# Kernel tuning notes

Hardware: AMD Instinct MI355X
Metric: run time of the kernel (lower is better)

The kernel has to match this reference:

```python
import jax, jax.numpy as jnp
import numpy as np

B, T, D_MODEL, H, RPR_K = 2, 2048, 1024, 16, 8
DK = D_MODEL // H  # 64
NUM_RPR = 2 * RPR_K + 1


def setup_inputs() -> dict:
    key = jax.random.key(0)
    ks = jax.random.split(key, 16)
    s = 0.02
    inp = {
        "query": jax.random.normal(ks[0], (B, T, D_MODEL), jnp.float32),
        "key": jax.random.normal(ks[1], (B, T, D_MODEL), jnp.float32),
        "value": jax.random.normal(ks[2], (B, T, D_MODEL), jnp.float32),
        "mask": jnp.ones((B, 1, 1, T), dtype=bool),
        "w_q": jax.random.normal(ks[3], (D_MODEL, H * DK), jnp.float32) * s,
        "b_q": jnp.zeros((H * DK,), jnp.float32),
        "w_k": jax.random.normal(ks[4], (D_MODEL, H * DK), jnp.float32) * s,
        "b_k": jnp.zeros((H * DK,), jnp.float32),
        "w_v": jax.random.normal(ks[5], (D_MODEL, H * DK), jnp.float32) * s,
        "b_v": jnp.zeros((H * DK,), jnp.float32),
        "w_o": jax.random.normal(ks[6], (H * DK, D_MODEL), jnp.float32) * s,
        "b_o": jnp.zeros((D_MODEL,), jnp.float32),
        "rpr_key_table": jax.random.normal(ks[7], (NUM_RPR, DK), jnp.float32),
        "rpr_value_table": jax.random.normal(ks[8], (NUM_RPR, DK), jnp.float32),
    }
    return inp


def _rel_edges(seq_len):
    # edges[i, j] = clamp(j - i + rpr_k, 0, 2*rpr_k)  -> [T, T] int32
    seq = jnp.arange(seq_len)
    edges = seq[None, :] - seq[:, None] + RPR_K
    return jnp.clip(edges, 0, 2 * RPR_K)


def reference(query, key, value, mask, w_q, b_q, w_k, b_k, w_v, b_v,
              w_o, b_o, rpr_key_table, rpr_value_table):
    Bsz, Tlen, _ = query.shape
    edges = _rel_edges(Tlen)                       # [T, T]
    ek = rpr_key_table[edges]                      # [T, T, DK]
    ev = rpr_value_table[edges]                    # [T, T, DK]

    def proj(x, w, b):
        return (x @ w + b).reshape(Bsz, Tlen, H, DK).transpose(0, 2, 1, 3)  # [B,H,T,DK]

    q = proj(query, w_q, b_q)
    k = proj(key, w_k, b_k)
    v = proj(value, w_v, b_v)

    scores_qk = jnp.einsum('bhtd,bhsd->bhts', q, k)
    scores_qek = jnp.einsum('bhtd,tsd->bhts', q, ek)
    scores = (scores_qk + scores_qek) / jnp.sqrt(jnp.float32(DK))
    scores = jnp.where(mask, scores, jnp.float32(-1e9))
    a = jax.nn.softmax(scores, axis=-1)            # [B,H,T,T]

    upd = jnp.einsum('bhts,bhsd->bhtd', a, v)
    upd_e = jnp.einsum('bhts,tsd->bhtd', a, ev)
    x = (upd + upd_e).transpose(0, 2, 1, 3).reshape(Bsz, Tlen, H * DK)
    return x @ w_o + b_o
```

## Files before the change

### kernel.cpp

```cpp
#include <hip/hip_runtime.h>
#include <stdint.h>


typedef unsigned short u16;
typedef __attribute__((ext_vector_type(4))) float f32x4;
typedef __attribute__((ext_vector_type(4))) int   i32x4;
typedef __attribute__((ext_vector_type(8))) __bf16 bh8;
typedef __attribute__((ext_vector_type(4))) __bf16 bh4;

#define T_LEN 2048
#define NHEAD 16
#define NR    17

#define SCALE_LOG2 0.18033688011112042f
#define CLAMP_LOG2 86.56170245333781f

__device__ __forceinline__ float bf2f(u16 x) {
  unsigned u = ((unsigned)x) << 16;
  return __builtin_bit_cast(float, u);
}
__device__ __forceinline__ u16 f2bf(float f) {
  unsigned u = __builtin_bit_cast(unsigned, f);
  u = u + 0x7fffu + ((u >> 16) & 1u);
  return (u16)(u >> 16);
}
__device__ __forceinline__ f32x4 zero4() { f32x4 z = {0.f, 0.f, 0.f, 0.f}; return z; }

__device__ __forceinline__ f32x4 mfma16(bh8 a, bh8 b, f32x4 c) {
  return __builtin_amdgcn_mfma_f32_16x16x32_bf16(a, b, c, 0, 0, 0);
}

__device__ __forceinline__ void bar_sync() {
  __builtin_amdgcn_sched_barrier(0);
  asm volatile("s_waitcnt lgkmcnt(0)" ::: "memory");
  __builtin_amdgcn_s_barrier();
  __builtin_amdgcn_sched_barrier(0);
}

__device__ __forceinline__ void wait_vm0() {
  __builtin_amdgcn_sched_barrier(0);
  asm volatile("s_waitcnt vmcnt(0)" ::: "memory");
  __builtin_amdgcn_sched_barrier(0);
}

__device__ __forceinline__ void async16(const u16* g, u16* l) {
  __builtin_amdgcn_global_load_lds(
      (const __attribute__((address_space(1))) void*)g,
      (__attribute__((address_space(3))) void*)l, 16, 0, 0);
}

__device__ __forceinline__ bh8 ldfrag(const u16* base, int row, int qc) {
  const i32x4 v = *(const i32x4*)(base + row * 64 + ((qc ^ (row & 7)) << 3));
  return __builtin_bit_cast(bh8, v);
}

__global__ __launch_bounds__(256) void prep_kernel(
    const float* __restrict__ xq, const float* __restrict__ xk,
    const float* __restrict__ xv, const float* __restrict__ w0,
    const float* __restrict__ w1, const float* __restrict__ w2,
    const float* __restrict__ w3, u16* __restrict__ oq, u16* __restrict__ ok,
    u16* __restrict__ ov, u16* __restrict__ t0, u16* __restrict__ t1,
    u16* __restrict__ t2, u16* __restrict__ t3) {
  __shared__ u16 tile[32][33];
  const int z = blockIdx.z;
  if (z < 3) {
    const float* S = (z == 0) ? xq : (z == 1) ? xk : xv;
    u16* D = (z == 0) ? oq : (z == 1) ? ok : ov;
    const size_t i = ((size_t)blockIdx.x * 256 + threadIdx.x) * 8;
    const f32x4 v0 = *(const f32x4*)(S + i);
    const f32x4 v1 = *(const f32x4*)(S + i + 4);
    u16 o[8];
#pragma unroll
    for (int j = 0; j < 4; ++j) {
      o[j] = f2bf(v0[j]);
      o[4 + j] = f2bf(v1[j]);
    }
    i32x4 w;
    __builtin_memcpy(&w, o, 16);
    *(i32x4*)(D + i) = w;
  } else {
    if (blockIdx.x >= 1024) return;
    const float* S = (z == 3) ? w0 : (z == 4) ? w1 : (z == 5) ? w2 : w3;
    u16* D = (z == 3) ? t0 : (z == 4) ? t1 : (z == 5) ? t2 : t3;
    const int tx = threadIdx.x & 31, ty = threadIdx.x >> 5;
    const int bx = blockIdx.x & 31, by = blockIdx.x >> 5;
#pragma unroll
    for (int i = 0; i < 4; ++i) {
      const int y = by * 32 + ty + i * 8;
      tile[ty + i * 8][tx] = f2bf(S[(size_t)y * 1024 + bx * 32 + tx]);
    }
    __syncthreads();
#pragma unroll
    for (int i = 0; i < 4; ++i) {
      const int y = bx * 32 + ty + i * 8;
      D[(size_t)y * 1024 + by * 32 + tx] = tile[tx][ty + i * 8];
    }
  }
}

__device__ __forceinline__ void gemm_body(const u16* __restrict__ A,
                                          const u16* __restrict__ Bm,
                                          const float* __restrict__ bias,
                                          void* __restrict__ out, int mode,
                                          int bm, int bn) {
  __shared__ __align__(16) u16 As[2][128 * 32];
  __shared__ __align__(16) u16 Bs[2][128 * 32];
  const int tid = threadIdx.x;
  const int wv = tid >> 6;
  const int ln = tid & 63;
  const int quad = ln >> 4, l15 = ln & 15;
  const int wr = wv >> 1, wc = wv & 1;

  f32x4 acc[4][4];
#pragma unroll
  for (int i = 0; i < 4; ++i)
#pragma unroll
    for (int j = 0; j < 4; ++j) acc[i][j] = zero4();

  const int c0 = tid, c1 = tid + 256;
  const size_t aoff0 = (size_t)(bm * 128 + (c0 >> 2)) * 1024 + (c0 & 3) * 8;
  const size_t aoff1 = (size_t)(bm * 128 + (c1 >> 2)) * 1024 + (c1 & 3) * 8;
  const size_t boff0 = (size_t)(bn * 128 + (c0 >> 2)) * 1024 + (c0 & 3) * 8;
  const size_t boff1 = (size_t)(bn * 128 + (c1 >> 2)) * 1024 + (c1 & 3) * 8;

  u16* ad0[2] = {&As[0][(wv * 64) * 8], &As[1][(wv * 64) * 8]};
  u16* ad1[2] = {&As[0][(256 + wv * 64) * 8], &As[1][(256 + wv * 64) * 8]};
  u16* bd0[2] = {&Bs[0][(wv * 64) * 8], &Bs[1][(wv * 64) * 8]};
  u16* bd1[2] = {&Bs[0][(256 + wv * 64) * 8], &Bs[1][(256 + wv * 64) * 8]};

  async16(A + aoff0, ad0[0]);
  async16(A + aoff1, ad1[0]);
  async16(Bm + boff0, bd0[0]);
  async16(Bm + boff1, bd1[0]);
  __syncthreads();

  for (int kt = 0; kt < 32; ++kt) {
    const int cur = kt & 1, nxt = cur ^ 1;
    if (kt < 31) {
      const int ko = (kt + 1) * 32;
      async16(A + aoff0 + ko, ad0[nxt]);
      async16(A + aoff1 + ko, ad1[nxt]);
      async16(Bm + boff0 + ko, bd0[nxt]);
      async16(Bm + boff1 + ko, bd1[nxt]);
    }

    bh8 af[4], bf[4];
#pragma unroll
    for (int mi = 0; mi < 4; ++mi)
      af[mi] = __builtin_bit_cast(
          bh8,
          *(const i32x4*)&As[cur][(wr * 64 + mi * 16 + l15) * 32 + quad * 8]);
#pragma unroll
    for (int ni = 0; ni < 4; ++ni)
      bf[ni] = __builtin_bit_cast(
          bh8,
          *(const i32x4*)&Bs[cur][(wc * 64 + ni * 16 + l15) * 32 + quad * 8]);
#pragma unroll
    for (int mi = 0; mi < 4; ++mi)
#pragma unroll
      for (int ni = 0; ni < 4; ++ni)
        acc[mi][ni] = mfma16(af[mi], bf[ni], acc[mi][ni]);

    __syncthreads();
  }

#pragma unroll
  for (int mi = 0; mi < 4; ++mi) {
    const int row0 = bm * 128 + wr * 64 + mi * 16 + quad * 4;
#pragma unroll
    for (int ni = 0; ni < 4; ++ni) {
      const int col = bn * 128 + wc * 64 + ni * 16 + l15;
      const float bcol = (mode == 3) ? 0.f : bias[col];
#pragma unroll
      for (int reg = 0; reg < 4; ++reg) {
        const int r = row0 + reg;
        const float v = acc[mi][ni][reg] + ((mode == 3) ? bias[r] : bcol);
        if (mode == 0) {
          ((float*)out)[(size_t)r * 1024 + col] = v;
        } else if (mode == 1) {
          const int bb = r >> 11, t = r & 2047;
          const int h = col >> 6, d = col & 63;
          ((u16*)out)[(((size_t)bb * NHEAD + h) * T_LEN + (size_t)t) * 64 + d] =
              f2bf(v);
        } else {
          const int h = r >> 6, d = r & 63;
          const int bb = col >> 11, t = col & 2047;
          ((u16*)out)[(((size_t)bb * NHEAD + h) * 64 + (size_t)d) * T_LEN + t] =
              f2bf(v);
        }
      }
    }
  }
}

__global__ __launch_bounds__(256) void gemm_qkv_kernel(
    const u16* __restrict__ xq, const u16* __restrict__ xk,
    const u16* __restrict__ xv, const u16* __restrict__ wtq,
    const u16* __restrict__ wtk, const u16* __restrict__ wtv,
    const float* __restrict__ bq, const float* __restrict__ bk,
    const float* __restrict__ bv, u16* __restrict__ oq, u16* __restrict__ ok,
    u16* __restrict__ ovt) {
  const int z = blockIdx.z;
  if (z == 0)
    gemm_body(xq, wtq, bq, oq, 1, blockIdx.x, blockIdx.y);
  else if (z == 1)
    gemm_body(xk, wtk, bk, ok, 1, blockIdx.x, blockIdx.y);
  else
    gemm_body(wtv, xv, bv, ovt, 3, blockIdx.y, blockIdx.x);
}

__global__ __launch_bounds__(256) void gemm_o_kernel(const u16* __restrict__ X,
                                                     const u16* __restrict__ Wt,
                                                     const float* __restrict__ bias,
                                                     float* __restrict__ out) {
  gemm_body(X, Wt, bias, out, 0, blockIdx.x, blockIdx.y);
}

__global__ __launch_bounds__(512) void attn_kernel(
    const u16* __restrict__ Qw, const u16* __restrict__ Kw,
    const u16* __restrict__ Vtw, const float* __restrict__ rkt,
    const float* __restrict__ rvt, u16* __restrict__ U) {
  __shared__ __align__(16) u16 smu[24576];
  __shared__ float smf[5120];
  u16* Qs = smu;
  u16* Ps = smu;
  float* qes = smf;
  float* aw = smf + 2176;
  float* lp = smf + 4352;
  float* s0p = smf + 4608;
  float* s16p = smf + 4864;
  float* rvs = (float*)(smu + 16384);

  const int tid = threadIdx.x;
  const int wv = tid >> 6, ln = tid & 63;
  const int tg = wv & 3, sh = wv >> 2;
  const int quad = ln >> 4, l15 = ln & 15;
  const int wg = blockIdx.x;
  const int xcd = wg & 7;
  const int slot = wg >> 3;
  const int qt = slot & 15;
  const int bh = xcd * 4 + (slot >> 4);
  const size_t hb = (size_t)bh * (T_LEN * 64);

  const int kr = tid >> 3;
  const int kgp = (tid & 7) ^ ((tid >> 3) & 7);
  const u16* ksrc = Kw + hb + (size_t)kr * 64 + kgp * 8;
  const u16* vsrc = Vtw + hb + (size_t)kr * T_LEN + kgp * 8;
  u16* const ldsK = smu + 8192 + wv * 512;
  u16* const ldsV = smu + 16384 + wv * 512;
  const int qrow = wv * 16 + ((ln >> 3) & 7);
  const int qgp = (ln & 7) ^ ((ln >> 3) & 7);
  const u16* qsrc = Qw + hb + (size_t)(qt * 128 + qrow) * 64 + qgp * 8;
  u16* const ldsQ = smu + wv * 1024;

  async16(qsrc, ldsQ);
  async16(qsrc + 512, ldsQ + 512);
  async16(ksrc, ldsK);
  async16(vsrc, ldsV);
  wait_vm0();
  bar_sync();

  for (int i = tid; i < 128 * NR; i += 512) {
    const int row = i / NR, r = i - row * NR;
    float s = 0.f;
#pragma unroll
    for (int c = 0; c < 8; ++c) {
      const i32x4 qv = *(const i32x4*)&Qs[row * 64 + ((c ^ (row & 7)) << 3)];
      const u16* qq = (const u16*)&qv;
#pragma unroll
      for (int j = 0; j < 8; ++j) s += bf2f(qq[j]) * rkt[r * 64 + c * 8 + j];
    }
    qes[i] = s;
    aw[i] = 0.f;
  }

  bh8 qf[2][2];
  const int row0 = tg * 32 + l15;
#pragma unroll
  for (int tt = 0; tt < 2; ++tt) {
    qf[tt][0] = ldfrag(Qs, row0 + tt * 16, quad);
    qf[tt][1] = ldfrag(Qs, row0 + tt * 16, quad + 4);
  }
  bar_sync();

  float qb0[2], qb16[2];
#pragma unroll
  for (int tt = 0; tt < 2; ++tt) {
    qb0[tt] = qes[(row0 + tt * 16) * NR + 0] * SCALE_LOG2;
    qb16[tt] = qes[(row0 + tt * 16) * NR + 16] * SCALE_LOG2;
  }

  float l_l[2] = {0.f, 0.f}, s0_l[2] = {0.f, 0.f}, s16_l[2] = {0.f, 0.f};
  f32x4 oacc[2][2];
#pragma unroll
  for (int tt = 0; tt < 2; ++tt)
#pragma unroll
    for (int ni = 0; ni < 2; ++ni) oacc[tt][ni] = zero4();

  for (int st = 0; st < 32; ++st) {
    const int cur = st & 1;
    const u16* Kc = smu + 8192 + cur * 4096;
    const u16* Vc = smu + 16384 + cur * 4096;
    if (st < 31) {
      const int nxt = cur ^ 1;
      async16(ksrc + (size_t)(st + 1) * 4096, ldsK + nxt * 4096);
      async16(vsrc + (size_t)(st + 1) * 64, ldsV + nxt * 4096);
    }

    __builtin_amdgcn_s_setprio(1);
#pragma unroll
    for (int m2 = 0; m2 < 2; ++m2) {
      const int srow = (sh * 2 + m2) * 16 + l15;
      const bh8 kf0 = ldfrag(Kc, srow, quad);
      const bh8 kf1 = ldfrag(Kc, srow, quad + 4);
#pragma unroll
      for (int tt = 0; tt < 2; ++tt) {
        f32x4 sacc = mfma16(kf0, qf[tt][0], zero4());
        sacc = mfma16(kf1, qf[tt][1], sacc);

        const int row = row0 + tt * 16;
        const int delta16 = st * 4 + sh * 2 + m2 - (qt * 8 + tg * 2 + tt);
        float p[4];
        if (delta16 < -1 || delta16 > 1) {
          const float qb = (delta16 < 0) ? qb0[tt] : qb16[tt];
          float ts = 0.f;
#pragma unroll
          for (int reg = 0; reg < 4; ++reg) {
            const float x = fminf(sacc[reg] * SCALE_LOG2 + qb, CLAMP_LOG2);
            const float pv = __builtin_amdgcn_exp2f(x);
            p[reg] = pv;
            ts += pv;
          }
          l_l[tt] += ts;
          if (delta16 < 0)
            s0_l[tt] += ts;
          else
            s16_l[tt] += ts;
        } else {
          const int base8 = delta16 * 16 + quad * 4 - l15 + 8;
#pragma unroll
          for (int reg = 0; reg < 4; ++reg) {
            int rel = base8 + reg;
            rel = rel < 0 ? 0 : (rel > 16 ? 16 : rel);
            const float x =
                fminf((sacc[reg] + qes[row * NR + rel]) * SCALE_LOG2,
                      CLAMP_LOG2);
            const float pv = __builtin_amdgcn_exp2f(x);
            p[reg] = pv;
            l_l[tt] += pv;
            if (rel == 0)
              s0_l[tt] += pv;
            else if (rel == 16)
              s16_l[tt] += pv;
            else
              atomicAdd(&aw[row * NR + rel], pv);
          }
        }

        bh4 pb = {(__bf16)p[0], (__bf16)p[1], (__bf16)p[2], (__bf16)p[3]};
        const int qc = 4 * sh + 2 * m2 + (quad >> 1);
        *(unsigned long long*)&Ps[row * 64 + ((qc ^ (row & 7)) << 3) +
                                  (quad & 1) * 4] =
            __builtin_bit_cast(unsigned long long, pb);
      }
    }

    bar_sync();

#pragma unroll
    for (int ks = 0; ks < 2; ++ks) {
      const int kc = ks * 4 + quad;
      const bh8 pf0 = ldfrag(Ps, row0, kc);
      const bh8 pf1 = ldfrag(Ps, row0 + 16, kc);
#pragma unroll
      for (int ni = 0; ni < 2; ++ni) {
        const bh8 vf = ldfrag(Vc, sh * 32 + ni * 16 + l15, kc);
        oacc[0][ni] = mfma16(pf0, vf, oacc[0][ni]);
        oacc[1][ni] = mfma16(pf1, vf, oacc[1][ni]);
      }
    }
    __builtin_amdgcn_s_setprio(0);

    wait_vm0();
    bar_sync();
  }

#pragma unroll
  for (int tt = 0; tt < 2; ++tt) {
    l_l[tt] += __shfl_xor(l_l[tt], 16);
    l_l[tt] += __shfl_xor(l_l[tt], 32);
    s0_l[tt] += __shfl_xor(s0_l[tt], 16);
    s0_l[tt] += __shfl_xor(s0_l[tt], 32);
    s16_l[tt] += __shfl_xor(s16_l[tt], 16);
    s16_l[tt] += __shfl_xor(s16_l[tt], 32);
    if (quad == 0) {
      lp[sh * 128 + row0 + tt * 16] = l_l[tt];
      s0p[sh * 128 + row0 + tt * 16] = s0_l[tt];
      s16p[sh * 128 + row0 + tt * 16] = s16_l[tt];
    }
  }
  for (int i = tid; i < NR * 64; i += 512) rvs[i] = rvt[i];
  __syncthreads();

  for (int i = tid; i < 128 * NR; i += 512) {
    const int row = i / NR, rr = i - row * NR;
    float v = aw[i];
    if (rr == 0) v += s0p[row] + s0p[128 + row];
    if (rr == 16) v += s16p[row] + s16p[128 + row];
    aw[i] = v;
  }
  if (tid < 128) lp[tid] += lp[128 + tid];
  __syncthreads();

  const int bb = bh >> 4, hh = bh & 15;
#pragma unroll
  for (int tt = 0; tt < 2; ++tt) {
#pragma unroll
    for (int ni = 0; ni < 2; ++ni) {
      const int d = sh * 32 + ni * 16 + l15;
#pragma unroll
      for (int reg = 0; reg < 4; ++reg) {
        const int rowi = tg * 32 + tt * 16 + quad * 4 + reg;
        float o = oacc[tt][ni][reg];
        float e = 0.f;
#pragma unroll
        for (int rr = 0; rr < NR; ++rr)
          e += aw[rowi * NR + rr] * rvs[rr * 64 + d];
        const float ov = (o + e) / lp[rowi];
        const int tgl = qt * 128 + rowi;
        U[((size_t)bb * T_LEN + tgl) * 1024 + hh * 64 + d] = f2bf(ov);
      }
    }
  }
}

extern "C" void kernel_launch(void* const* d_in, const int* in_sizes, int n_in,
                              void* d_out, int out_size, void* d_ws,
                              size_t ws_size, hipStream_t stream) {
  const float* query = (const float*)d_in[0];
  const float* key = (const float*)d_in[1];
  const float* value = (const float*)d_in[2];
  const float* w_q = (const float*)d_in[4];
  const float* b_q = (const float*)d_in[5];
  const float* w_k = (const float*)d_in[6];
  const float* b_k = (const float*)d_in[7];
  const float* w_v = (const float*)d_in[8];
  const float* b_v = (const float*)d_in[9];
  const float* w_o = (const float*)d_in[10];
  const float* b_o = (const float*)d_in[11];
  const float* rkt = (const float*)d_in[12];
  const float* rvt = (const float*)d_in[13];

  char* ws = (char*)d_ws;
  const size_t MB2 = 1u << 21, MB8 = 1u << 23;
  u16* wtq = (u16*)(ws + 0 * MB2);
  u16* wtk = (u16*)(ws + 1 * MB2);
  u16* wtv = (u16*)(ws + 2 * MB2);
  u16* wto = (u16*)(ws + 3 * MB2);
  u16* Xq = (u16*)(ws + 4 * MB2 + 0 * MB8);
  u16* Xk = (u16*)(ws + 4 * MB2 + 1 * MB8);
  u16* Xv = (u16*)(ws + 4 * MB2 + 2 * MB8);
  u16* Qw = (u16*)(ws + 4 * MB2 + 3 * MB8);
  u16* Kw = (u16*)(ws + 4 * MB2 + 4 * MB8);
  u16* Vtw = (u16*)(ws + 4 * MB2 + 5 * MB8);
  u16* Uw = (u16*)(ws + 4 * MB2 + 6 * MB8);

  prep_kernel<<<dim3(2048, 1, 7), 256, 0, stream>>>(
      query, key, value, w_q, w_k, w_v, w_o, Xq, Xk, Xv, wtq, wtk, wtv, wto);
  gemm_qkv_kernel<<<dim3(32, 8, 3), 256, 0, stream>>>(
      Xq, Xk, Xv, wtq, wtk, wtv, b_q, b_k, b_v, Qw, Kw, Vtw);
  attn_kernel<<<dim3(512), 512, 0, stream>>>(Qw, Kw, Vtw, rkt, rvt, Uw);
  gemm_o_kernel<<<dim3(32, 8), 256, 0, stream>>>(Uw, wto, b_o, (float*)d_out);
}
```

Measured before the change: 315.4 us.

## Restructure attention to 32x32 MFMA with register-resident P via permlane swap

The attention kernel moves from 512 threads using 16x16x32 MFMAs to 256 threads where each wave owns 32 query rows and computes the full 64-wide key block with 32x32x16 MFMAs. P is converted to bf16 with packed converts and rearranged across lane halves with v_permlane32_swap, so it feeds the PV MFMA directly from registers. This removes the LDS round trip for P and the mid-iteration barrier, and the cross-wave reduction of row sums. In exchange there are fewer waves per block, larger accumulators (more VGPR pressure) and more reliance on LDS async loads per wave.

```diff
diff --git a/kernel.cpp b/kernel.cpp
--- a/kernel.cpp
+++ b/kernel.cpp
@@ -4,9 +4,9 @@
 
 typedef unsigned short u16;
 typedef __attribute__((ext_vector_type(4))) float f32x4;
+typedef __attribute__((ext_vector_type(16))) float f32x16;
 typedef __attribute__((ext_vector_type(4))) int   i32x4;
 typedef __attribute__((ext_vector_type(8))) __bf16 bh8;
-typedef __attribute__((ext_vector_type(4))) __bf16 bh4;
 
 #define T_LEN 2048
 #define NHEAD 16
@@ -25,9 +25,23 @@
   return (u16)(u >> 16);
 }
 __device__ __forceinline__ f32x4 zero4() { f32x4 z = {0.f, 0.f, 0.f, 0.f}; return z; }
+__device__ __forceinline__ f32x16 zero16() {
+  f32x16 z = {0.f, 0.f, 0.f, 0.f, 0.f, 0.f, 0.f, 0.f,
+              0.f, 0.f, 0.f, 0.f, 0.f, 0.f, 0.f, 0.f};
+  return z;
+}
 
 __device__ __forceinline__ f32x4 mfma16(bh8 a, bh8 b, f32x4 c) {
   return __builtin_amdgcn_mfma_f32_16x16x32_bf16(a, b, c, 0, 0, 0);
+}
+__device__ __forceinline__ f32x16 mfma32(bh8 a, bh8 b, f32x16 c) {
+  return __builtin_amdgcn_mfma_f32_32x32x16_bf16(a, b, c, 0, 0, 0);
+}
+
+__device__ __forceinline__ unsigned cvtpk(float a, float b) {
+  unsigned r;
+  asm("v_cvt_pk_bf16_f32 %0, %1, %2" : "=v"(r) : "v"(a), "v"(b));
+  return r;
 }
 
 __device__ __forceinline__ void bar_sync() {
@@ -216,51 +230,55 @@
   gemm_body(X, Wt, bias, out, 0, blockIdx.x, blockIdx.y);
 }
 
-__global__ __launch_bounds__(512) void attn_kernel(
+__global__ __launch_bounds__(256) void attn_kernel(
     const u16* __restrict__ Qw, const u16* __restrict__ Kw,
     const u16* __restrict__ Vtw, const float* __restrict__ rkt,
     const float* __restrict__ rvt, u16* __restrict__ U) {
   __shared__ __align__(16) u16 smu[24576];
-  __shared__ float smf[5120];
-  u16* Qs = smu;
-  u16* Ps = smu;
-  float* qes = smf;
-  float* aw = smf + 2176;
-  float* lp = smf + 4352;
-  float* s0p = smf + 4608;
-  float* s16p = smf + 4864;
-  float* rvs = (float*)(smu + 16384);
+  __shared__ float smf[5568];
+  u16* const Qs = smu;
+  float* const qes = smf;
+  float* const aw = smf + 2176;
+  float* const lp = smf + 4352;
+  float* const rvs = smf + 4480;
 
   const int tid = threadIdx.x;
   const int wv = tid >> 6, ln = tid & 63;
-  const int tg = wv & 3, sh = wv >> 2;
-  const int quad = ln >> 4, l15 = ln & 15;
+  const int l31 = ln & 31, hi = ln >> 5;
   const int wg = blockIdx.x;
   const int xcd = wg & 7;
   const int slot = wg >> 3;
   const int qt = slot & 15;
   const int bh = xcd * 4 + (slot >> 4);
   const size_t hb = (size_t)bh * (T_LEN * 64);
-
-  const int kr = tid >> 3;
-  const int kgp = (tid & 7) ^ ((tid >> 3) & 7);
-  const u16* ksrc = Kw + hb + (size_t)kr * 64 + kgp * 8;
-  const u16* vsrc = Vtw + hb + (size_t)kr * T_LEN + kgp * 8;
-  u16* const ldsK = smu + 8192 + wv * 512;
-  u16* const ldsV = smu + 16384 + wv * 512;
-  const int qrow = wv * 16 + ((ln >> 3) & 7);
-  const int qgp = (ln & 7) ^ ((ln >> 3) & 7);
-  const u16* qsrc = Qw + hb + (size_t)(qt * 128 + qrow) * 64 + qgp * 8;
-  u16* const ldsQ = smu + wv * 1024;
-
-  async16(qsrc, ldsQ);
-  async16(qsrc + 512, ldsQ + 512);
-  async16(ksrc, ldsK);
-  async16(vsrc, ldsV);
+  const int t0 = qt * 128 + wv * 32;
+  const int tl = wv * 32 + l31;
+
+  const int r8 = ln >> 3, c8 = ln & 7;
+  const int kgp = c8 ^ (r8 & 7);
+  const u16* ksrc0 = Kw + hb + (size_t)(wv * 16 + r8) * 64 + kgp * 8;
+  const u16* ksrc1 = Kw + hb + (size_t)(wv * 16 + 8 + r8) * 64 + kgp * 8;
+  const u16* vsrc0 = Vtw + hb + (size_t)(wv * 16 + r8) * T_LEN + kgp * 8;
+  const u16* vsrc1 = Vtw + hb + (size_t)(wv * 16 + 8 + r8) * T_LEN + kgp * 8;
+  u16* const ldsK0 = smu + 8192 + (wv * 16) * 64;
+  u16* const ldsK1 = smu + 8192 + (wv * 16 + 8) * 64;
+  u16* const ldsV0 = smu + 16384 + (wv * 16) * 64;
+  u16* const ldsV1 = smu + 16384 + (wv * 16 + 8) * 64;
+
+  {
+    const u16* qsrc = Qw + hb + (size_t)(qt * 128 + wv * 32 + r8) * 64 + kgp * 8;
+#pragma unroll
+    for (int a = 0; a < 4; ++a)
+      async16(qsrc + (size_t)(a * 8) * 64, Qs + (wv * 32 + a * 8) * 64);
+  }
+  async16(ksrc0, ldsK0);
+  async16(ksrc1, ldsK1);
+  async16(vsrc0, ldsV0);
+  async16(vsrc1, ldsV1);
   wait_vm0();
   bar_sync();
 
-  for (int i = tid; i < 128 * NR; i += 512) {
+  for (int i = tid; i < 128 * NR; i += 256) {
     const int row = i / NR, r = i - row * NR;
     float s = 0.f;
 #pragma unroll
@@ -273,29 +291,16 @@
     qes[i] = s;
     aw[i] = 0.f;
   }
-
-  bh8 qf[2][2];
-  const int row0 = tg * 32 + l15;
-#pragma unroll
-  for (int tt = 0; tt < 2; ++tt) {
-    qf[tt][0] = ldfrag(Qs, row0 + tt * 16, quad);
-    qf[tt][1] = ldfrag(Qs, row0 + tt * 16, quad + 4);
-  }
   bar_sync();
 
-  float qb0[2], qb16[2];
-#pragma unroll
-  for (int tt = 0; tt < 2; ++tt) {
-    qb0[tt] = qes[(row0 + tt * 16) * NR + 0] * SCALE_LOG2;
-    qb16[tt] = qes[(row0 + tt * 16) * NR + 16] * SCALE_LOG2;
-  }
-
-  float l_l[2] = {0.f, 0.f}, s0_l[2] = {0.f, 0.f}, s16_l[2] = {0.f, 0.f};
-  f32x4 oacc[2][2];
-#pragma unroll
-  for (int tt = 0; tt < 2; ++tt)
-#pragma unroll
-    for (int ni = 0; ni < 2; ++ni) oacc[tt][ni] = zero4();
+  const float qb0 = qes[tl * NR + 0] * SCALE_LOG2;
+  const float qb16 = qes[tl * NR + 16] * SCALE_LOG2;
+  bh8 qf[4];
+#pragma unroll
+  for (int kb = 0; kb < 4; ++kb) qf[kb] = ldfrag(Qs, tl, kb * 2 + hi);
+
+  float l_l = 0.f, s0_l = 0.f, s16_l = 0.f;
+  f32x16 oacc[2] = {zero16(), zero16()};
 
   for (int st = 0; st < 32; ++st) {
     const int cur = st & 1;
@@ -303,80 +308,82 @@
     const u16* Vc = smu + 16384 + cur * 4096;
     if (st < 31) {
       const int nxt = cur ^ 1;
-      async16(ksrc + (size_t)(st + 1) * 4096, ldsK + nxt * 4096);
-      async16(vsrc + (size_t)(st + 1) * 64, ldsV + nxt * 4096);
-    }
-
+      async16(ksrc0 + (size_t)(st + 1) * 4096, ldsK0 + nxt * 4096);
+      async16(ksrc1 + (size_t)(st + 1) * 4096, ldsK1 + nxt * 4096);
+      async16(vsrc0 + (size_t)(st + 1) * 64, ldsV0 + nxt * 4096);
+      async16(vsrc1 + (size_t)(st + 1) * 64, ldsV1 + nxt * 4096);
+    }
     __builtin_amdgcn_s_setprio(1);
-#pragma unroll
-    for (int m2 = 0; m2 < 2; ++m2) {
-      const int srow = (sh * 2 + m2) * 16 + l15;
-      const bh8 kf0 = ldfrag(Kc, srow, quad);
-      const bh8 kf1 = ldfrag(Kc, srow, quad + 4);
-#pragma unroll
-      for (int tt = 0; tt < 2; ++tt) {
-        f32x4 sacc = mfma16(kf0, qf[tt][0], zero4());
-        sacc = mfma16(kf1, qf[tt][1], sacc);
-
-        const int row = row0 + tt * 16;
-        const int delta16 = st * 4 + sh * 2 + m2 - (qt * 8 + tg * 2 + tt);
-        float p[4];
-        if (delta16 < -1 || delta16 > 1) {
-          const float qb = (delta16 < 0) ? qb0[tt] : qb16[tt];
-          float ts = 0.f;
-#pragma unroll
-          for (int reg = 0; reg < 4; ++reg) {
-            const float x = fminf(sacc[reg] * SCALE_LOG2 + qb, CLAMP_LOG2);
-            const float pv = __builtin_amdgcn_exp2f(x);
-            p[reg] = pv;
-            ts += pv;
-          }
-          l_l[tt] += ts;
-          if (delta16 < 0)
-            s0_l[tt] += ts;
+
+#pragma unroll
+    for (int sb = 0; sb < 2; ++sb) {
+      f32x16 sacc = zero16();
+#pragma unroll
+      for (int kb = 0; kb < 4; ++kb) {
+        const bh8 kf = ldfrag(Kc, sb * 32 + l31, kb * 2 + hi);
+        sacc = mfma32(kf, qf[kb], sacc);
+      }
+
+      const int sbase = st * 64 + sb * 32;
+      float p[16];
+      if (sbase + 39 <= t0) {
+        float ts = 0.f;
+#pragma unroll
+        for (int r = 0; r < 16; ++r) {
+          const float x = fminf(sacc[r] * SCALE_LOG2 + qb0, CLAMP_LOG2);
+          const float pv = __builtin_amdgcn_exp2f(x);
+          p[r] = pv;
+          ts += pv;
+        }
+        l_l += ts;
+        s0_l += ts;
+      } else if (sbase >= t0 + 39) {
+        float ts = 0.f;
+#pragma unroll
+        for (int r = 0; r < 16; ++r) {
+          const float x = fminf(sacc[r] * SCALE_LOG2 + qb16, CLAMP_LOG2);
+          const float pv = __builtin_amdgcn_exp2f(x);
+          p[r] = pv;
+          ts += pv;
+        }
+        l_l += ts;
+        s16_l += ts;
+      } else {
+        const int base = sbase + 4 * hi - (t0 + l31) + 8;
+#pragma unroll
+        for (int r = 0; r < 16; ++r) {
+          int rel = base + (r & 3) + 8 * (r >> 2);
+          rel = rel < 0 ? 0 : (rel > 16 ? 16 : rel);
+          const float x = fminf((sacc[r] + qes[tl * NR + rel]) * SCALE_LOG2,
+                                CLAMP_LOG2);
+          const float pv = __builtin_amdgcn_exp2f(x);
+          p[r] = pv;
+          l_l += pv;
+          if (rel == 0)
+            s0_l += pv;
+          else if (rel == 16)
+            s16_l += pv;
           else
-            s16_l[tt] += ts;
-        } else {
-          const int base8 = delta16 * 16 + quad * 4 - l15 + 8;
-#pragma unroll
-          for (int reg = 0; reg < 4; ++reg) {
-            int rel = base8 + reg;
-            rel = rel < 0 ? 0 : (rel > 16 ? 16 : rel);
-            const float x =
-                fminf((sacc[reg] + qes[row * NR + rel]) * SCALE_LOG2,
-                      CLAMP_LOG2);
-            const float pv = __builtin_amdgcn_exp2f(x);
-            p[reg] = pv;
-            l_l[tt] += pv;
-            if (rel == 0)
-              s0_l[tt] += pv;
-            else if (rel == 16)
-              s16_l[tt] += pv;
-            else
-              atomicAdd(&aw[row * NR + rel], pv);
-          }
+            atomicAdd(&aw[tl * NR + rel], pv);
         }
-
-        bh4 pb = {(__bf16)p[0], (__bf16)p[1], (__bf16)p[2], (__bf16)p[3]};
-        const int qc = 4 * sh + 2 * m2 + (quad >> 1);
-        *(unsigned long long*)&Ps[row * 64 + ((qc ^ (row & 7)) << 3) +
-                                  (quad & 1) * 4] =
-            __builtin_bit_cast(unsigned long long, pb);
       }
-    }
-
-    bar_sync();
-
-#pragma unroll
-    for (int ks = 0; ks < 2; ++ks) {
-      const int kc = ks * 4 + quad;
-      const bh8 pf0 = ldfrag(Ps, row0, kc);
-      const bh8 pf1 = ldfrag(Ps, row0 + 16, kc);
-#pragma unroll
-      for (int ni = 0; ni < 2; ++ni) {
-        const bh8 vf = ldfrag(Vc, sh * 32 + ni * 16 + l15, kc);
-        oacc[0][ni] = mfma16(pf0, vf, oacc[0][ni]);
-        oacc[1][ni] = mfma16(pf1, vf, oacc[1][ni]);
+
+#pragma unroll
+      for (int h = 0; h < 2; ++h) {
+        unsigned wa = cvtpk(p[8 * h + 0], p[8 * h + 1]);
+        unsigned wb = cvtpk(p[8 * h + 2], p[8 * h + 3]);
+        unsigned wc = cvtpk(p[8 * h + 4], p[8 * h + 5]);
+        unsigned wd = cvtpk(p[8 * h + 6], p[8 * h + 7]);
+        asm("v_permlane32_swap_b32 %0, %1" : "+v"(wa), "+v"(wc));
+        asm("v_permlane32_swap_b32 %0, %1" : "+v"(wb), "+v"(wd));
+        const i32x4 fr = {(int)wa, (int)wb, (int)wc, (int)wd};
+        const bh8 pa = __builtin_bit_cast(bh8, fr);
+        const int ks = sb * 2 + h;
+#pragma unroll
+        for (int db = 0; db < 2; ++db) {
+          const bh8 vf = ldfrag(Vc, db * 32 + l31, ks * 2 + hi);
+          oacc[db] = mfma32(pa, vf, oacc[db]);
+        }
       }
     }
     __builtin_amdgcn_s_setprio(0);
@@ -385,52 +392,35 @@
     bar_sync();
   }
 
-#pragma unroll
-  for (int tt = 0; tt < 2; ++tt) {
-    l_l[tt] += __shfl_xor(l_l[tt], 16);
-    l_l[tt] += __shfl_xor(l_l[tt], 32);
-    s0_l[tt] += __shfl_xor(s0_l[tt], 16);
-    s0_l[tt] += __shfl_xor(s0_l[tt], 32);
-    s16_l[tt] += __shfl_xor(s16_l[tt], 16);
-    s16_l[tt] += __shfl_xor(s16_l[tt], 32);
-    if (quad == 0) {
-      lp[sh * 128 + row0 + tt * 16] = l_l[tt];
-      s0p[sh * 128 + row0 + tt * 16] = s0_l[tt];
-      s16p[sh * 128 + row0 + tt * 16] = s16_l[tt];
-    }
-  }
-  for (int i = tid; i < NR * 64; i += 512) rvs[i] = rvt[i];
+  l_l += __shfl_xor(l_l, 32);
+  s0_l += __shfl_xor(s0_l, 32);
+  s16_l += __shfl_xor(s16_l, 32);
+  if (ln < 32) lp[tl] = l_l;
+  for (int i = tid; i < NR * 64; i += 256) rvs[i] = rvt[i];
   __syncthreads();
-
-  for (int i = tid; i < 128 * NR; i += 512) {
-    const int row = i / NR, rr = i - row * NR;
-    float v = aw[i];
-    if (rr == 0) v += s0p[row] + s0p[128 + row];
-    if (rr == 16) v += s16p[row] + s16p[128 + row];
-    aw[i] = v;
-  }
-  if (tid < 128) lp[tid] += lp[128 + tid];
+  if (ln < 32) {
+    aw[tl * NR + 0] += s0_l;
+    aw[tl * NR + 16] += s16_l;
+  }
   __syncthreads();
 
   const int bb = bh >> 4, hh = bh & 15;
 #pragma unroll
-  for (int tt = 0; tt < 2; ++tt) {
-#pragma unroll
-    for (int ni = 0; ni < 2; ++ni) {
-      const int d = sh * 32 + ni * 16 + l15;
-#pragma unroll
-      for (int reg = 0; reg < 4; ++reg) {
-        const int rowi = tg * 32 + tt * 16 + quad * 4 + reg;
-        float o = oacc[tt][ni][reg];
-        float e = 0.f;
-#pragma unroll
-        for (int rr = 0; rr < NR; ++rr)
-          e += aw[rowi * NR + rr] * rvs[rr * 64 + d];
-        const float ov = (o + e) / lp[rowi];
-        const int tgl = qt * 128 + rowi;
-        U[((size_t)bb * T_LEN + tgl) * 1024 + hh * 64 + d] = f2bf(ov);
-      }
-    }
+  for (int r = 0; r < 16; ++r) {
+    const int srow = (r & 3) + 8 * (r >> 2) + 4 * hi;
+    const int trow = wv * 32 + srow;
+    const float linv = 1.f / lp[trow];
+    float e0 = 0.f, e1 = 0.f;
+#pragma unroll
+    for (int rr = 0; rr < NR; ++rr) {
+      const float awv = aw[trow * NR + rr];
+      e0 += awv * rvs[rr * 64 + l31];
+      e1 += awv * rvs[rr * 64 + 32 + l31];
+    }
+    const int tg = qt * 128 + trow;
+    const size_t ubase = ((size_t)bb * T_LEN + tg) * 1024 + hh * 64;
+    U[ubase + l31] = f2bf((oacc[0][r] + e0) * linv);
+    U[ubase + 32 + l31] = f2bf((oacc[1][r] + e1) * linv);
   }
 }
 
@@ -469,6 +459,6 @@
       query, key, value, w_q, w_k, w_v, w_o, Xq, Xk, Xv, wtq, wtk, wtv, wto);
   gemm_qkv_kernel<<<dim3(32, 8, 3), 256, 0, stream>>>(
       Xq, Xk, Xv, wtq, wtk, wtv, b_q, b_k, b_v, Qw, Kw, Vtw);
-  attn_kernel<<<dim3(512), 512, 0, stream>>>(Qw, Kw, Vtw, rkt, rvt, Uw);
+  attn_kernel<<<dim3(512), 256, 0, stream>>>(Qw, Kw, Vtw, rkt, rvt, Uw);
   gemm_o_kernel<<<dim3(32, 8), 256, 0, stream>>>(Uw, wto, b_o, (float*)d_out);
 }
```

Result: faster. 283.1 us (-10.2%).
